# Kernel optimization log

Hardware: AMD Instinct MI355X
Metric: run time of the kernel (lower is better)

## Reference

```python
import jax, jax.numpy as jnp
import numpy as np

B, N, C, W = 256, 4096, 16, 10
L = N - W + 1
EPS = 1e-5


def setup_inputs() -> dict:
    key = jax.random.key(0)
    ks = jax.random.split(key, 6)
    def lin(k, shape, fan_in):
        # mimic nn.Linear default init scale ~ U(-1/sqrt(fan), 1/sqrt(fan))
        b = 1.0 / np.sqrt(fan_in)
        return jax.random.uniform(k, shape, jnp.float32, -b, b)
    return {
        "x": jax.random.normal(ks[0], (B, N, C, 2), jnp.float32),
        "W_in_real": lin(ks[1], (C, L), L),      # per-channel input filter (real)
        "W_in_imag": lin(ks[2], (C, L), L),      # per-channel input filter (imag)
        "W_nl": lin(ks[3], (C, 2, 2 * C), 2 * C),  # per-channel Linear(2C -> 2)
        "W_out_real": lin(ks[4], (C, W), W),      # per-channel output filter (real)
        "W_out_imag": lin(ks[5], (C, W), W),      # per-channel output filter (imag)
        "gamma": jnp.ones((C,), jnp.float32),     # BatchNorm1d weight
        "beta": jnp.zeros((C,), jnp.float32),     # BatchNorm1d bias
    }


def _depthwise_valid(x_bcn, w_cl):
    # sliding dot-products f[:, c, id] = sum_l x[:, c, id+l] * w[c, l]
    # == depthwise 1D valid correlation: [B,C,N] * [C,L] -> [B,C,W]
    nC = w_cl.shape[0]
    return jax.lax.conv_general_dilated(
        x_bcn, w_cl[:, None, :], window_strides=(1,), padding='VALID',
        dimension_numbers=('NCH', 'OIH', 'NCH'), feature_group_count=nC)


def reference(x, W_in_real, W_in_imag, W_nl, W_out_real, W_out_imag, gamma, beta):
    xr = jnp.transpose(x[..., 0], (0, 2, 1))  # [B,C,N]
    xi = jnp.transpose(x[..., 1], (0, 2, 1))
    # stage 1: per-channel windowed filters + amplitude (|f|^2) scaling
    fr = jnp.transpose(_depthwise_valid(xr, W_in_real), (0, 2, 1))  # [B,W,C]
    fi = jnp.transpose(_depthwise_valid(xi, W_in_imag), (0, 2, 1))  # [B,W,C]
    amp = fr * fr + fi * fi
    fr = amp * fr
    fi = amp * fi
    # stage 2: per-channel nonlin Linear(2C -> 2) on cat([real, imag])
    tf = jnp.concatenate([fr, fi], axis=-1)            # [B,W,2C]
    nl = jnp.einsum('bwi,coi->bwco', tf, W_nl)         # [B,W,C,2]
    nr, ni = nl[..., 0], nl[..., 1]                    # [B,W,C]
    # stage 3: per-channel output filters over the out_window dim
    out_r = jnp.einsum('bwc,cw->bc', nr, W_out_real)   # [B,C]
    out_i = jnp.einsum('bwc,cw->bc', ni, W_out_imag)   # [B,C]
    out = jnp.stack([out_r, out_i], axis=-1)           # [B,C,2]
    # BatchNorm1d(n_channels) in training mode: stats over (batch, last) per channel
    mean = out.mean(axis=(0, 2), keepdims=True)
    var = out.var(axis=(0, 2), keepdims=True)
    return (out - mean) / jnp.sqrt(var + EPS) * gamma[None, :, None] + beta[None, :, None]
```

## Files before the change

### kernel.cpp

```cpp
#include <hip/hip_runtime.h>

#define BB 256
#define NN 4096
#define CC 16
#define WW 10
#define LL 4087
#define EPSF 1e-5f

#define GLOAD16(gsrc, ldst)                                                                  \
    __builtin_amdgcn_global_load_lds((const __attribute__((address_space(1))) void*)(gsrc),  \
                                     (__attribute__((address_space(3))) void*)(ldst), 16, 0, 0)

__global__ __launch_bounds__(256) void pack_weights(const float* __restrict__ Wr,
                                                    const float* __restrict__ Wi,
                                                    float2* __restrict__ pk) {
    int tg = blockIdx.x * 256 + threadIdx.x;
    int n = tg >> 4, c = tg & 15;
    float2 v = make_float2(0.f, 0.f);
    if (n < LL) { v.x = Wr[c * LL + n]; v.y = Wi[c * LL + n]; }
    pk[tg] = v;
}

__global__ __launch_bounds__(1024, 4) void fused_pipe(const float* __restrict__ x,
                                                      const float2* __restrict__ pk,
                                                      const float* __restrict__ Wnl,
                                                      const float* __restrict__ Wor,
                                                      const float* __restrict__ Woi,
                                                      float* __restrict__ outraw) {
    __shared__ __align__(16) char smem[131072];

    const int b = blockIdx.x;
    const int tid = threadIdx.x;
    const int c = tid & 15;
    const int tc = tid >> 4;
    const int base = tc * 2;
    const int lane = tid & 63, wave = tid >> 6;

    const char* __restrict__ xsrc =
        (const char*)x + (size_t)b * (NN * CC * 8) + wave * 1024 + lane * 16;
    const char* __restrict__ psrc = (const char*)pk + wave * 1024 + lane * 16;

#define STAGE(u)                                                            \
    do {                                                                    \
        GLOAD16(xsrc + (size_t)(u) * 16384,                                 \
                smem + ((u) & 3) * 16384 + wave * 1024);                    \
        GLOAD16(psrc + (size_t)(u) * 16384,                                 \
                smem + 65536 + ((u) & 3) * 16384 + wave * 1024);            \
    } while (0)

    float fr[WW], fi[WW];
#pragma unroll
    for (int w = 0; w < WW; ++w) { fr[w] = 0.f; fi[w] = 0.f; }

    STAGE(0);
    STAGE(1);
    if (tid < 288) ((float*)(smem + 65536 + 3 * 16384 + 119 * 128))[tid] = 0.f;
    asm volatile("s_waitcnt lgkmcnt(0)" ::: "memory");

#pragma unroll 1
    for (int t = 0; t < 32; ++t) {
        if (t < 31) {
            asm volatile("s_waitcnt vmcnt(2)" ::: "memory");
        } else {
            asm volatile("s_waitcnt vmcnt(0)" ::: "memory");
        }
        __builtin_amdgcn_s_barrier();
        __builtin_amdgcn_sched_barrier(0);

        if (t + 2 < 32) STAGE(t + 2);

        const float2* __restrict__ xb = (const float2*)(smem + (t & 3) * 16384);
        const float2* __restrict__ pc = (const float2*)(smem + 65536 + (t & 3) * 16384);
        const float2* __restrict__ pp = (const float2*)(smem + 65536 + ((t + 3) & 3) * 16384);

        float2 wv[11];
#pragma unroll
        for (int k = 0; k < 11; ++k) {
            const int r = base + k - 9;
            const float2* __restrict__ sp =
                (r < 0) ? (pp + ((r + 128) * 16 + c)) : (pc + (r * 16 + c));
            wv[k] = *sp;
        }
        const float2 xv0 = xb[base * 16 + c];
        const float2 xv1 = xb[(base + 1) * 16 + c];
#pragma unroll
        for (int w = 0; w < WW; ++w) {
            fr[w] += xv0.x * wv[9 - w].x;
            fi[w] += xv0.y * wv[9 - w].y;
            fr[w] += xv1.x * wv[10 - w].x;
            fi[w] += xv1.y * wv[10 - w].y;
        }
    }
#undef STAGE

#pragma unroll
    for (int w = 0; w < WW; ++w) {
        fr[w] += __shfl_xor(fr[w], 16);
        fr[w] += __shfl_xor(fr[w], 32);
        fi[w] += __shfl_xor(fi[w], 16);
        fi[w] += __shfl_xor(fi[w], 32);
    }
    float (*red)[320] = (float (*)[320])smem;
    float* F2 = (float*)(smem + 20480);
    float* nls = (float*)(smem + 21760);
    if (lane < 16) {
#pragma unroll
        for (int w = 0; w < WW; ++w) {
            red[wave][lane * 20 + w] = fr[w];
            red[wave][lane * 20 + 10 + w] = fi[w];
        }
    }
    __syncthreads();
    if (tid < 320) {
        float s = 0.f;
#pragma unroll
        for (int k = 0; k < 16; ++k) s += red[k][tid];
        F2[tid] = s;
    }
    __syncthreads();
    if (tid < 160) {
        const int cc = tid / 10, w = tid % 10;
        const float a = F2[cc * 20 + w], q = F2[cc * 20 + 10 + w];
        const float amp = a * a + q * q;
        F2[cc * 20 + w] = a * amp;
        F2[cc * 20 + 10 + w] = q * amp;
    }
    __syncthreads();
    if (tid < 320) {
        const int cc = tid / 20, rem = tid % 20, o = rem / 10, w = rem % 10;
        const float* __restrict__ wn = Wnl + (cc * 2 + o) * 32;
        float acc = 0.f;
#pragma unroll
        for (int i = 0; i < 16; ++i) acc += F2[i * 20 + w] * wn[i];
#pragma unroll
        for (int i = 0; i < 16; ++i) acc += F2[i * 20 + 10 + w] * wn[16 + i];
        nls[tid] = acc;
    }
    __syncthreads();
    if (tid < 32) {
        const int cc = tid >> 1, o = tid & 1;
        const float* __restrict__ wo = (o == 0 ? Wor : Woi) + cc * WW;
        float acc = 0.f;
#pragma unroll
        for (int w = 0; w < WW; ++w) acc += nls[cc * 20 + o * 10 + w] * wo[w];
        outraw[b * 32 + cc * 2 + o] = acc;
    }
}

__global__ __launch_bounds__(1024, 4) void fused_main_nopk(const float* __restrict__ x,
                                                           const float* __restrict__ Wr,
                                                           const float* __restrict__ Wi,
                                                           const float* __restrict__ Wnl,
                                                           const float* __restrict__ Wor,
                                                           const float* __restrict__ Woi,
                                                           float* __restrict__ outraw) {
    const int b = blockIdx.x;
    const int tid = threadIdx.x;
    const int tc = tid >> 4;
    const int c = tid & 15;
    const int n0 = tc * 64;

    const float2* __restrict__ x2 = (const float2*)x + (size_t)b * (NN * CC) + (n0 * 16 + c);

    float tr[9], ti[9];
    float fr[WW], fi[WW];
#pragma unroll
    for (int w = 0; w < WW; ++w) { fr[w] = 0.f; fi[w] = 0.f; }

#pragma unroll
    for (int j = 0; j < 9; ++j) {
        const int m = n0 - 9 + j;
        const int mc = m < 0 ? 0 : m;
        const float a = Wr[c * LL + mc], q = Wi[c * LL + mc];
        tr[j] = (m >= 0) ? a : 0.f;
        ti[j] = (m >= 0) ? q : 0.f;
    }

#pragma unroll 1
    for (int g = 0; g < 4; ++g) {
        const int nb = n0 + g * 16;
        float2 xb[16], wb[16];
#pragma unroll
        for (int p = 0; p < 16; ++p) {
            xb[p] = x2[p * 16];
            const int n = nb + p;
            const int nc2 = (n < LL) ? n : (LL - 1);
            const float a = Wr[c * LL + nc2], q = Wi[c * LL + nc2];
            wb[p].x = (n < LL) ? a : 0.f;
            wb[p].y = (n < LL) ? q : 0.f;
        }
        x2 += 256;
#pragma unroll
        for (int p = 0; p < 16; ++p) {
#pragma unroll
            for (int w = 0; w < WW; ++w) {
                const int q = p - w;
                const float wr_ = (q >= 0) ? wb[q].x : tr[q + 9];
                const float wi_ = (q >= 0) ? wb[q].y : ti[q + 9];
                fr[w] += xb[p].x * wr_;
                fi[w] += xb[p].y * wi_;
            }
        }
#pragma unroll
        for (int j = 0; j < 9; ++j) { tr[j] = wb[j + 7].x; ti[j] = wb[j + 7].y; }
    }

#pragma unroll
    for (int w = 0; w < WW; ++w) {
        fr[w] += __shfl_xor(fr[w], 16);
        fr[w] += __shfl_xor(fr[w], 32);
        fi[w] += __shfl_xor(fi[w], 16);
        fi[w] += __shfl_xor(fi[w], 32);
    }
    __shared__ float red[16][320];
    __shared__ float F2[320];
    __shared__ float nls[320];
    const int lane = tid & 63, wave = tid >> 6;
    if (lane < 16) {
#pragma unroll
        for (int w = 0; w < WW; ++w) {
            red[wave][lane * 20 + w] = fr[w];
            red[wave][lane * 20 + 10 + w] = fi[w];
        }
    }
    __syncthreads();
    if (tid < 320) {
        float s = 0.f;
#pragma unroll
        for (int k = 0; k < 16; ++k) s += red[k][tid];
        F2[tid] = s;
    }
    __syncthreads();
    if (tid < 160) {
        const int cc = tid / 10, w = tid % 10;
        const float a = F2[cc * 20 + w], q = F2[cc * 20 + 10 + w];
        const float amp = a * a + q * q;
        F2[cc * 20 + w] = a * amp;
        F2[cc * 20 + 10 + w] = q * amp;
    }
    __syncthreads();
    if (tid < 320) {
        const int cc = tid / 20, rem = tid % 20, o = rem / 10, w = rem % 10;
        const float* __restrict__ wn = Wnl + (cc * 2 + o) * 32;
        float acc = 0.f;
#pragma unroll
        for (int i = 0; i < 16; ++i) acc += F2[i * 20 + w] * wn[i];
#pragma unroll
        for (int i = 0; i < 16; ++i) acc += F2[i * 20 + 10 + w] * wn[16 + i];
        nls[tid] = acc;
    }
    __syncthreads();
    if (tid < 32) {
        const int cc = tid >> 1, o = tid & 1;
        const float* __restrict__ wo = (o == 0 ? Wor : Woi) + cc * WW;
        float acc = 0.f;
#pragma unroll
        for (int w = 0; w < WW; ++w) acc += nls[cc * 20 + o * 10 + w] * wo[w];
        outraw[b * 32 + cc * 2 + o] = acc;
    }
}

__global__ __launch_bounds__(256) void bnorm(float* __restrict__ out,
                                             const float* __restrict__ gamma,
                                             const float* __restrict__ beta) {
    const int c = blockIdx.x;
    const int t = threadIdx.x;
    const float v0 = out[t * 32 + c * 2 + 0];
    const float v1 = out[t * 32 + c * 2 + 1];
    float s = v0 + v1;
    float ss = v0 * v0 + v1 * v1;
#pragma unroll
    for (int off = 32; off > 0; off >>= 1) {
        s += __shfl_down(s, off, 64);
        ss += __shfl_down(ss, off, 64);
    }
    __shared__ float ls[8];
    const int wave = t >> 6, lane = t & 63;
    if (lane == 0) { ls[wave * 2] = s; ls[wave * 2 + 1] = ss; }
    __syncthreads();
    const float S = ls[0] + ls[2] + ls[4] + ls[6];
    const float SS = ls[1] + ls[3] + ls[5] + ls[7];
    const float mean = S * (1.f / 512.f);
    const float var = SS * (1.f / 512.f) - mean * mean;
    const float scale = gamma[c] * rsqrtf(var + EPSF);
    const float sh = beta[c];
    out[t * 32 + c * 2 + 0] = (v0 - mean) * scale + sh;
    out[t * 32 + c * 2 + 1] = (v1 - mean) * scale + sh;
}

extern "C" void kernel_launch(void* const* d_in, const int* in_sizes, int n_in,
                              void* d_out, int out_size, void* d_ws, size_t ws_size,
                              hipStream_t stream) {
    const float* x     = (const float*)d_in[0];
    const float* Wr    = (const float*)d_in[1];
    const float* Wi    = (const float*)d_in[2];
    const float* Wnl   = (const float*)d_in[3];
    const float* Wor   = (const float*)d_in[4];
    const float* Woi   = (const float*)d_in[5];
    const float* gamma = (const float*)d_in[6];
    const float* beta  = (const float*)d_in[7];
    float* out = (float*)d_out;

    const size_t pk_bytes = (size_t)NN * CC * sizeof(float2);
    float2* pk = (float2*)d_ws;
    const bool use_pk = (ws_size >= pk_bytes);

    if (use_pk) {
        hipLaunchKernelGGL(pack_weights, dim3(256), dim3(256), 0, stream, Wr, Wi, pk);
        hipLaunchKernelGGL(fused_pipe, dim3(BB), dim3(1024), 0, stream,
                           x, pk, Wnl, Wor, Woi, out);
    } else {
        hipLaunchKernelGGL(fused_main_nopk, dim3(BB), dim3(1024), 0, stream,
                           x, Wr, Wi, Wnl, Wor, Woi, out);
    }
    hipLaunchKernelGGL(bnorm, dim3(CC), dim3(256), 0, stream, out, gamma, beta);
}
```

Baseline: 217.0 us.

## Split fused pipeline into register-blocked stage1 across 1024 blocks plus epilogue kernel

Replaces the LDS-staged, barrier-synchronised 1024-thread fused kernel with a 256-thread stage1 kernel that splits each batch across four blocks. Each thread reads x and the packed weights directly from global memory into registers, carrying a 9-tap halo between chunks. Per-wave partial sums go to a workspace buffer, and a separate epilogue kernel reduces them and applies the amplitude, nonlinear and output-filter steps. The aim is to drop the LDS double-buffering and per-iteration barriers and to raise block-level parallelism. The cost is an extra kernel launch, a global round trip for the partials, and a larger workspace requirement that falls back to the old path when the workspace is too small.

```diff
diff --git a/kernel.cpp b/kernel.cpp
--- a/kernel.cpp
+++ b/kernel.cpp
@@ -6,10 +6,6 @@
 #define WW 10
 #define LL 4087
 #define EPSF 1e-5f
-
-#define GLOAD16(gsrc, ldst)                                                                  \
-    __builtin_amdgcn_global_load_lds((const __attribute__((address_space(1))) void*)(gsrc),  \
-                                     (__attribute__((address_space(3))) void*)(ldst), 16, 0, 0)
 
 __global__ __launch_bounds__(256) void pack_weights(const float* __restrict__ Wr,
                                                     const float* __restrict__ Wi,
@@ -21,77 +17,57 @@
     pk[tg] = v;
 }
 
-__global__ __launch_bounds__(1024, 4) void fused_pipe(const float* __restrict__ x,
-                                                      const float2* __restrict__ pk,
-                                                      const float* __restrict__ Wnl,
-                                                      const float* __restrict__ Wor,
-                                                      const float* __restrict__ Woi,
-                                                      float* __restrict__ outraw) {
-    __shared__ __align__(16) char smem[131072];
-
-    const int b = blockIdx.x;
+__global__ __launch_bounds__(256, 4) void stage1(const float* __restrict__ x,
+                                                 const float2* __restrict__ pk,
+                                                 float* __restrict__ fpart) {
+    const int bid = blockIdx.x;
+    const int b = bid >> 2, q = bid & 3;
     const int tid = threadIdx.x;
+    const int tc = tid >> 4;
     const int c = tid & 15;
-    const int tc = tid >> 4;
-    const int base = tc * 2;
-    const int lane = tid & 63, wave = tid >> 6;
-
-    const char* __restrict__ xsrc =
-        (const char*)x + (size_t)b * (NN * CC * 8) + wave * 1024 + lane * 16;
-    const char* __restrict__ psrc = (const char*)pk + wave * 1024 + lane * 16;
-
-#define STAGE(u)                                                            \
-    do {                                                                    \
-        GLOAD16(xsrc + (size_t)(u) * 16384,                                 \
-                smem + ((u) & 3) * 16384 + wave * 1024);                    \
-        GLOAD16(psrc + (size_t)(u) * 16384,                                 \
-                smem + 65536 + ((u) & 3) * 16384 + wave * 1024);            \
-    } while (0)
-
+    const int n0 = q * 1024 + tc * 64;
+
+    const float2* __restrict__ x2 = (const float2*)x + (size_t)b * (NN * CC) + (n0 * 16 + c);
+    const float2* __restrict__ pkp = pk + (n0 * 16 + c);
+
+    float tr[9], ti[9];
     float fr[WW], fi[WW];
 #pragma unroll
     for (int w = 0; w < WW; ++w) { fr[w] = 0.f; fi[w] = 0.f; }
 
-    STAGE(0);
-    STAGE(1);
-    if (tid < 288) ((float*)(smem + 65536 + 3 * 16384 + 119 * 128))[tid] = 0.f;
-    asm volatile("s_waitcnt lgkmcnt(0)" ::: "memory");
+#pragma unroll
+    for (int j = 0; j < 9; ++j) {
+        const int m = n0 - 9 + j;
+        float vr = 0.f, vi = 0.f;
+        if (m >= 0) { const float2 t = pk[m * 16 + c]; vr = t.x; vi = t.y; }
+        tr[j] = vr;
+        ti[j] = vi;
+    }
 
 #pragma unroll 1
-    for (int t = 0; t < 32; ++t) {
-        if (t < 31) {
-            asm volatile("s_waitcnt vmcnt(2)" ::: "memory");
-        } else {
-            asm volatile("s_waitcnt vmcnt(0)" ::: "memory");
-        }
-        __builtin_amdgcn_s_barrier();
-        __builtin_amdgcn_sched_barrier(0);
-
-        if (t + 2 < 32) STAGE(t + 2);
-
-        const float2* __restrict__ xb = (const float2*)(smem + (t & 3) * 16384);
-        const float2* __restrict__ pc = (const float2*)(smem + 65536 + (t & 3) * 16384);
-        const float2* __restrict__ pp = (const float2*)(smem + 65536 + ((t + 3) & 3) * 16384);
-
-        float2 wv[11];
-#pragma unroll
-        for (int k = 0; k < 11; ++k) {
-            const int r = base + k - 9;
-            const float2* __restrict__ sp =
-                (r < 0) ? (pp + ((r + 128) * 16 + c)) : (pc + (r * 16 + c));
-            wv[k] = *sp;
-        }
-        const float2 xv0 = xb[base * 16 + c];
-        const float2 xv1 = xb[(base + 1) * 16 + c];
-#pragma unroll
-        for (int w = 0; w < WW; ++w) {
-            fr[w] += xv0.x * wv[9 - w].x;
-            fi[w] += xv0.y * wv[9 - w].y;
-            fr[w] += xv1.x * wv[10 - w].x;
-            fi[w] += xv1.y * wv[10 - w].y;
-        }
-    }
-#undef STAGE
+    for (int g = 0; g < 4; ++g) {
+        float2 xb[16], wb[16];
+#pragma unroll
+        for (int p = 0; p < 16; ++p) {
+            xb[p] = x2[p * 16];
+            wb[p] = pkp[p * 16];
+        }
+        x2 += 256;
+        pkp += 256;
+#pragma unroll
+        for (int p = 0; p < 16; ++p) {
+#pragma unroll
+            for (int w = 0; w < WW; ++w) {
+                const int u = p - w;
+                const float wr_ = (u >= 0) ? wb[u].x : tr[u + 9];
+                const float wi_ = (u >= 0) ? wb[u].y : ti[u + 9];
+                fr[w] += xb[p].x * wr_;
+                fi[w] += xb[p].y * wi_;
+            }
+        }
+#pragma unroll
+        for (int j = 0; j < 9; ++j) { tr[j] = wb[j + 7].x; ti[j] = wb[j + 7].y; }
+    }
 
 #pragma unroll
     for (int w = 0; w < WW; ++w) {
@@ -100,33 +76,42 @@
         fi[w] += __shfl_xor(fi[w], 16);
         fi[w] += __shfl_xor(fi[w], 32);
     }
-    float (*red)[320] = (float (*)[320])smem;
-    float* F2 = (float*)(smem + 20480);
-    float* nls = (float*)(smem + 21760);
+    const int lane = tid & 63, wave = tid >> 6;
     if (lane < 16) {
+        float* __restrict__ dst = fpart + (size_t)(bid * 4 + wave) * 320 + lane * 20;
 #pragma unroll
         for (int w = 0; w < WW; ++w) {
-            red[wave][lane * 20 + w] = fr[w];
-            red[wave][lane * 20 + 10 + w] = fi[w];
-        }
-    }
-    __syncthreads();
-    if (tid < 320) {
-        float s = 0.f;
-#pragma unroll
-        for (int k = 0; k < 16; ++k) s += red[k][tid];
-        F2[tid] = s;
-    }
+            dst[w] = fr[w];
+            dst[10 + w] = fi[w];
+        }
+    }
+}
+
+__global__ __launch_bounds__(320) void epilogue(const float* __restrict__ fpart,
+                                                const float* __restrict__ Wnl,
+                                                const float* __restrict__ Wor,
+                                                const float* __restrict__ Woi,
+                                                float* __restrict__ outraw) {
+    const int b = blockIdx.x;
+    const int tid = threadIdx.x;
+    __shared__ float F2[320];
+    __shared__ float nls[320];
+
+    float s = 0.f;
+    const float* __restrict__ fp = fpart + (size_t)b * 16 * 320 + tid;
+#pragma unroll
+    for (int k = 0; k < 16; ++k) s += fp[k * 320];
+    F2[tid] = s;
     __syncthreads();
     if (tid < 160) {
         const int cc = tid / 10, w = tid % 10;
-        const float a = F2[cc * 20 + w], q = F2[cc * 20 + 10 + w];
-        const float amp = a * a + q * q;
+        const float a = F2[cc * 20 + w], qq = F2[cc * 20 + 10 + w];
+        const float amp = a * a + qq * qq;
         F2[cc * 20 + w] = a * amp;
-        F2[cc * 20 + 10 + w] = q * amp;
-    }
-    __syncthreads();
-    if (tid < 320) {
+        F2[cc * 20 + 10 + w] = qq * amp;
+    }
+    __syncthreads();
+    {
         const int cc = tid / 20, rem = tid % 20, o = rem / 10, w = rem % 10;
         const float* __restrict__ wn = Wnl + (cc * 2 + o) * 32;
         float acc = 0.f;
@@ -194,9 +179,9 @@
         for (int p = 0; p < 16; ++p) {
 #pragma unroll
             for (int w = 0; w < WW; ++w) {
-                const int q = p - w;
-                const float wr_ = (q >= 0) ? wb[q].x : tr[q + 9];
-                const float wi_ = (q >= 0) ? wb[q].y : ti[q + 9];
+                const int u = p - w;
+                const float wr_ = (u >= 0) ? wb[u].x : tr[u + 9];
+                const float wi_ = (u >= 0) ? wb[u].y : ti[u + 9];
                 fr[w] += xb[p].x * wr_;
                 fi[w] += xb[p].y * wi_;
             }
@@ -302,13 +287,16 @@
     float* out = (float*)d_out;
 
     const size_t pk_bytes = (size_t)NN * CC * sizeof(float2);
+    const size_t fp_bytes = (size_t)4096 * 320 * sizeof(float);
     float2* pk = (float2*)d_ws;
-    const bool use_pk = (ws_size >= pk_bytes);
-
-    if (use_pk) {
+    float* fpart = (float*)((char*)d_ws + pk_bytes);
+    const bool use_ws = (ws_size >= pk_bytes + fp_bytes);
+
+    if (use_ws) {
         hipLaunchKernelGGL(pack_weights, dim3(256), dim3(256), 0, stream, Wr, Wi, pk);
-        hipLaunchKernelGGL(fused_pipe, dim3(BB), dim3(1024), 0, stream,
-                           x, pk, Wnl, Wor, Woi, out);
+        hipLaunchKernelGGL(stage1, dim3(1024), dim3(256), 0, stream, x, pk, fpart);
+        hipLaunchKernelGGL(epilogue, dim3(BB), dim3(320), 0, stream,
+                           fpart, Wnl, Wor, Woi, out);
     } else {
         hipLaunchKernelGGL(fused_main_nopk, dim3(BB), dim3(1024), 0, stream,
                            x, Wr, Wi, Wnl, Wor, Woi, out);
```

After: 212.4 us. 2.1% less time.
